# Kernel optimization log

Hardware: AMD Instinct MI355X
Metric: run time of the kernel (lower is better)

## Reference

```python
import jax, jax.numpy as jnp
import numpy as np

H = 256      # hidden_size
B = 32       # batch
T = 4096     # timesteps / graph nodes
E = 8192     # edges per graph
PATH = 1
EXPAND_WEIGHT = 0.1
MODE = 'son'


def setup_inputs() -> dict:
    key = jax.random.key(0)
    ks = jax.random.split(key, 6)
    hidden = jax.random.normal(ks[0], (B, H), jnp.float32)
    encoder_outputs = jax.random.normal(ks[1], (T, B, H), jnp.float32)
    edges_src = jax.random.randint(ks[2], (B, E), 0, T)
    edges_dst = jax.random.randint(ks[3], (B, E), 0, T)
    # nn.Linear(2H, 2H) params (kaiming-uniform-ish scale) and the v vector
    lim = 1.0 / np.sqrt(2 * H)
    W_attn = jax.random.uniform(ks[4], (2 * H, 2 * H), jnp.float32, -lim, lim)
    b_attn = jnp.zeros((2 * H,), jnp.float32)
    v = jax.random.uniform(ks[5], (2 * H,), jnp.float32, -lim, lim)
    return {"hidden": hidden, "encoder_outputs": encoder_outputs,
            "edges_src": edges_src, "edges_dst": edges_dst,
            "W_attn": W_attn, "b_attn": b_attn, "v": v}


def reference(hidden, encoder_outputs, edges_src, edges_dst, W_attn, b_attn, v):
    Bb, Hh = hidden.shape
    Tt = encoder_outputs.shape[0]
    # h: [B, T, H] (hidden repeated over timesteps); enc: [B, T, H]
    h = jnp.broadcast_to(hidden[:, None, :], (Bb, Tt, Hh))
    enc = jnp.transpose(encoder_outputs, (1, 0, 2))
    # score: tanh(Linear(cat)) then v . energy -> [B, T]
    energy = jnp.tanh(jnp.concatenate([h, enc], axis=2) @ W_attn.T + b_attn)
    scores = jnp.einsum('btd,d->bt', energy, v)
    w = jax.nn.softmax(scores, axis=1)
    # expand_attn: scatter-add along graph edges, skipping consecutive (y == x+1)
    mask = (edges_dst != edges_src + 1).astype(w.dtype)  # [B, E]
    def scatter(wb, src, dst, m):
        if MODE == 'son':
            return jnp.zeros_like(wb).at[dst].add(wb[src] * m)
        else:
            return jnp.zeros_like(wb).at[src].add(wb[dst] * m)
    for _ in range(PATH):
        w = jax.vmap(scatter)(w, edges_src, edges_dst, mask) * EXPAND_WEIGHT
    return w[:, None, :]  # [B, 1, T]
```

## Files before the change

kernel.cpp:

```cpp
#include <hip/hip_runtime.h>
#include <hip/hip_bf16.h>

typedef __attribute__((ext_vector_type(8))) short bf16x8;
typedef __attribute__((ext_vector_type(4))) float f32x4;

#define HD 256
#define NB 32
#define NT 4096
#define NE 8192
#define N2 512

static __device__ __forceinline__ unsigned short f2bf(float f) {
  unsigned int u = __float_as_uint(f);
  u += 0x7fff + ((u >> 16) & 1);
  return (unsigned short)(u >> 16);
}
static __device__ __forceinline__ short4 cvt4(float4 a) {
  return make_short4((short)f2bf(a.x), (short)f2bf(a.y),
                     (short)f2bf(a.z), (short)f2bf(a.w));
}
static __device__ __forceinline__ float fast_tanh(float x) {
  float e = __builtin_amdgcn_exp2f(x * 2.8853900817779268f);
  return __builtin_fmaf(-2.f, __builtin_amdgcn_rcpf(e + 1.f), 1.f);
}
static __device__ __forceinline__ bf16x8 pack8(float4 a, float4 b) {
  union { bf16x8 v; unsigned int u[4]; } r;
  r.u[0] = (__float_as_uint(a.y) & 0xffff0000u) | (__float_as_uint(a.x) >> 16);
  r.u[1] = (__float_as_uint(a.w) & 0xffff0000u) | (__float_as_uint(a.z) >> 16);
  r.u[2] = (__float_as_uint(b.y) & 0xffff0000u) | (__float_as_uint(b.x) >> 16);
  r.u[3] = (__float_as_uint(b.w) & 0xffff0000u) | (__float_as_uint(b.z) >> 16);
  return r.v;
}

#define GLDS16(g, l)                                                       \
  __builtin_amdgcn_global_load_lds(                                        \
      (const __attribute__((address_space(1))) unsigned int*)(g),          \
      (__attribute__((address_space(3))) unsigned int*)(l), 16, 0, 0)

__global__ __launch_bounds__(256) void prep(
    const float* __restrict__ hidden, const float* __restrict__ Wattn,
    const float* __restrict__ battn, float* __restrict__ cvecT,
    short* __restrict__ Wbf) {
  const int tid = threadIdx.x;
  if (blockIdx.x < 256) {
    __shared__ float Ws[64 * 260];
    __shared__ float Hs[HD];
    const int chunk = blockIdx.x & 7;
    const int b = blockIdx.x >> 3;
#pragma unroll
    for (int it = 0; it < 16; ++it) {
      int f = it * 1024 + tid * 4;
      int i = f >> 8, k = f & 255;
      float4 w4 = *(const float4*)(Wattn + (chunk * 64 + i) * N2 + k);
      *(float4*)&Ws[i * 260 + k] = w4;
    }
    if (tid < 64)
      *(float4*)&Hs[tid * 4] = *(const float4*)(hidden + b * HD + tid * 4);
    __syncthreads();
    const int nl = tid >> 2;
    const int kb = (tid & 3) * 64;
    float sum = 0.f;
#pragma unroll
    for (int z = 0; z < 64; z += 4) {
      float4 h4 = *(const float4*)&Hs[kb + z];
      float4 w4 = *(const float4*)&Ws[nl * 260 + kb + z];
      sum = fmaf(h4.x, w4.x, sum);
      sum = fmaf(h4.y, w4.y, sum);
      sum = fmaf(h4.z, w4.z, sum);
      sum = fmaf(h4.w, w4.w, sum);
    }
    sum += __shfl_xor(sum, 1, 64);
    sum += __shfl_xor(sum, 2, 64);
    if ((tid & 3) == 0)
      cvecT[(chunk * 64 + nl) * NB + b] = sum + battn[chunk * 64 + nl];
  } else {
    int f = (blockIdx.x - 256) * 1024 + tid * 4;
    int n = f >> 8, k = f & 255;
    float4 w4 = *(const float4*)(Wattn + n * N2 + HD + k);
    *(short4*)(Wbf + f) = cvt4(w4);
  }
}

__global__ __launch_bounds__(256, 2) void score_gemm(
    const float* __restrict__ enc, const short* __restrict__ Wbf,
    const float* __restrict__ cvecT, const float* __restrict__ vvec,
    float* __restrict__ scores) {
  __shared__ float As[512 * 4];
  __shared__ short Bs[2048 * 8];
  __shared__ float part[4][64];
  const int tid = threadIdx.x;
  const int w = tid >> 6, lane = tid & 63, q = lane >> 4, m = lane & 15;
  const int row0 = blockIdx.x * 64;

  f32x4 acc[4][8];
#pragma unroll
  for (int mi = 0; mi < 4; ++mi)
#pragma unroll
    for (int nf = 0; nf < 8; ++nf) acc[mi][nf] = (f32x4){0.f, 0.f, 0.f, 0.f};

#pragma unroll 1
  for (int ks = 0; ks < 8; ++ks) {
    const int k0 = ks * 32;
    __syncthreads();
#pragma unroll
    for (int i = 0; i < 2; ++i) {
      const int S = (i * 4 + w) * 64 + lane;
      const int r = S >> 3;
      const int kc = (S & 7) ^ (r & 7);
      GLDS16(enc + (row0 + r) * HD + k0 + kc * 4, &As[(S & ~63) * 4]);
    }
#pragma unroll
    for (int i = 0; i < 8; ++i) {
      const int S = (i * 4 + w) * 64 + lane;
      const int n = S >> 2;
      const int kc = (S & 3) ^ ((n >> 1) & 3);
      GLDS16(Wbf + n * HD + k0 + kc * 8, &Bs[(S & ~63) * 8]);
    }
    __syncthreads();

    bf16x8 bfr[8];
#pragma unroll
    for (int nf = 0; nf < 8; ++nf) {
      const int n = w * 128 + nf * 16 + m;
      bfr[nf] = *(const bf16x8*)&Bs[(n * 4 + (q ^ ((n >> 1) & 3))) * 8];
    }
#pragma unroll
    for (int mi = 0; mi < 4; ++mi) {
      const int r = mi * 16 + m;
      float4 a0 = *(const float4*)&As[(r * 8 + ((2 * q) ^ (r & 7))) * 4];
      float4 a1 = *(const float4*)&As[(r * 8 + ((2 * q + 1) ^ (r & 7))) * 4];
      bf16x8 af = pack8(a0, a1);
#pragma unroll
      for (int nf = 0; nf < 8; ++nf)
        acc[mi][nf] = __builtin_amdgcn_mfma_f32_16x16x32_bf16(af, bfr[nf], acc[mi][nf], 0, 0, 0);
    }
  }

  float p[4][4];
#pragma unroll
  for (int mi = 0; mi < 4; ++mi)
#pragma unroll
    for (int j = 0; j < 4; ++j) p[mi][j] = 0.f;

#pragma unroll
  for (int nf = 0; nf < 8; ++nf) {
    const int n = w * 128 + nf * 16 + m;
    const float vv = vvec[n];
    const f32x4 cvA = *(const f32x4*)(cvecT + n * NB + 4 * q);
    const f32x4 cvB = *(const f32x4*)(cvecT + n * NB + 16 + 4 * q);
#pragma unroll
    for (int mi = 0; mi < 4; ++mi) {
      const f32x4 cv = (mi & 1) ? cvB : cvA;
#pragma unroll
      for (int j = 0; j < 4; ++j)
        p[mi][j] += fast_tanh(acc[mi][nf][j] + cv[j]) * vv;
    }
  }
#pragma unroll
  for (int mi = 0; mi < 4; ++mi) {
#pragma unroll
    for (int j = 0; j < 4; ++j) {
      float e = p[mi][j];
      e += __shfl_xor(e, 1, 64);
      e += __shfl_xor(e, 2, 64);
      e += __shfl_xor(e, 4, 64);
      e += __shfl_xor(e, 8, 64);
      if (m == 0) part[w][mi * 16 + 4 * q + j] = e;
    }
  }
  __syncthreads();
  if (tid < 64) {
    const int r = row0 + tid;
    scores[(r & 31) * NT + (r >> 5)] =
        part[0][tid] + part[1][tid] + part[2][tid] + part[3][tid];
  }
}

__global__ __launch_bounds__(1024) void softmax_norm(
    const float* __restrict__ sc, float* __restrict__ smax,
    float* __restrict__ sinv, float* __restrict__ out) {
  __shared__ float rtmp[16];
  __shared__ float rres;
  const int b = blockIdx.x;
  const int tid = threadIdx.x;
  const int wid = tid >> 6, lane = tid & 63;
  float s[4];
  float mx = -1e30f;
#pragma unroll
  for (int p = 0; p < 4; ++p) {
    s[p] = sc[b * NT + tid + p * 1024];
    mx = fmaxf(mx, s[p]);
  }
#pragma unroll
  for (int d = 32; d >= 1; d >>= 1) mx = fmaxf(mx, __shfl_xor(mx, d, 64));
  if (lane == 0) rtmp[wid] = mx;
  __syncthreads();
  if (tid == 0) {
    float mm = rtmp[0];
#pragma unroll
    for (int i = 1; i < 16; ++i) mm = fmaxf(mm, rtmp[i]);
    rres = mm;
  }
  __syncthreads();
  mx = rres;
  float sm = 0.f;
#pragma unroll
  for (int p = 0; p < 4; ++p) sm += __expf(s[p] - mx);
#pragma unroll
  for (int d = 32; d >= 1; d >>= 1) sm += __shfl_xor(sm, d, 64);
  if (lane == 0) rtmp[wid] = sm;
  __syncthreads();
  if (tid == 0) {
    float tt = 0.f;
#pragma unroll
    for (int i = 0; i < 16; ++i) tt += rtmp[i];
    smax[b] = mx;
    sinv[b] = 0.1f / tt;
  }
#pragma unroll
  for (int p = 0; p < 4; ++p) out[b * NT + tid + p * 1024] = 0.f;
}

__global__ __launch_bounds__(256) void scatter(
    const float* __restrict__ sc, const float* __restrict__ smax,
    const float* __restrict__ sinv, const int* __restrict__ esrc,
    const int* __restrict__ edst, float* __restrict__ out) {
  const int idx = blockIdx.x * 256 + threadIdx.x;
  const int b = idx >> 13, e = idx & (NE - 1);
  const int ss = esrc[b * NE + e];
  const int dd = edst[b * NE + e];
  const float wv = __expf(sc[b * NT + ss] - smax[b]) * sinv[b];
  if (dd != ss + 1) atomicAdd(out + b * NT + dd, wv);
}

extern "C" void kernel_launch(void* const* d_in, const int* in_sizes, int n_in,
                              void* d_out, int out_size, void* d_ws, size_t ws_size,
                              hipStream_t stream) {
  const float* hidden = (const float*)d_in[0];
  const float* enc    = (const float*)d_in[1];
  const int*   esrc   = (const int*)d_in[2];
  const int*   edst   = (const int*)d_in[3];
  const float* Wattn  = (const float*)d_in[4];
  const float* battn  = (const float*)d_in[5];
  const float* vvec   = (const float*)d_in[6];
  float* out = (float*)d_out;

  char* ws = (char*)d_ws;
  float* cvecT  = (float*)ws;
  short* Wbf    = (short*)(ws + 65536);
  float* scores = (float*)(ws + 65536 + 262144);
  float* smax   = (float*)(ws + 65536 + 262144 + 524288);
  float* sinv   = (float*)(ws + 65536 + 262144 + 524288 + 128);

  prep<<<384, 256, 0, stream>>>(hidden, Wattn, battn, cvecT, Wbf);
  score_gemm<<<(NB * NT) / 64, 256, 0, stream>>>(enc, Wbf, cvecT, vvec, scores);
  softmax_norm<<<NB, 1024, 0, stream>>>(scores, smax, sinv, out);
  scatter<<<(NB * NE) / 256, 256, 0, stream>>>(scores, smax, sinv, esrc, edst, out);
}
```

Measured before the change: 279.3 us.

## Stage full bf16 A tile in LDS once, stream W fragments from global

The score GEMM now loads the block's whole 64x256 encoder tile once, converts it to bf16 into swizzled shared memory, and drops the per-k-step LDS staging of both operands and the barriers between steps. W fragments are read straight from global memory (L2-resident) with a register double-buffer. The N dimension is split into two passes of 64 columns per wave, which halves the accumulator registers, and launch bounds are raised to allow three blocks per CU. The cost is more global and L2 traffic for W per block, plus a serialized upfront load of the encoder tile with no overlap against compute.

```diff
diff --git a/kernel.cpp b/kernel.cpp
--- a/kernel.cpp
+++ b/kernel.cpp
@@ -23,19 +23,6 @@
   float e = __builtin_amdgcn_exp2f(x * 2.8853900817779268f);
   return __builtin_fmaf(-2.f, __builtin_amdgcn_rcpf(e + 1.f), 1.f);
 }
-static __device__ __forceinline__ bf16x8 pack8(float4 a, float4 b) {
-  union { bf16x8 v; unsigned int u[4]; } r;
-  r.u[0] = (__float_as_uint(a.y) & 0xffff0000u) | (__float_as_uint(a.x) >> 16);
-  r.u[1] = (__float_as_uint(a.w) & 0xffff0000u) | (__float_as_uint(a.z) >> 16);
-  r.u[2] = (__float_as_uint(b.y) & 0xffff0000u) | (__float_as_uint(b.x) >> 16);
-  r.u[3] = (__float_as_uint(b.w) & 0xffff0000u) | (__float_as_uint(b.z) >> 16);
-  return r.v;
-}
-
-#define GLDS16(g, l)                                                       \
-  __builtin_amdgcn_global_load_lds(                                        \
-      (const __attribute__((address_space(1))) unsigned int*)(g),          \
-      (__attribute__((address_space(3))) unsigned int*)(l), 16, 0, 0)
 
 __global__ __launch_bounds__(256) void prep(
     const float* __restrict__ hidden, const float* __restrict__ Wattn,
@@ -81,86 +68,95 @@
   }
 }
 
-__global__ __launch_bounds__(256, 2) void score_gemm(
+__global__ __launch_bounds__(256, 3) void score_gemm(
     const float* __restrict__ enc, const short* __restrict__ Wbf,
     const float* __restrict__ cvecT, const float* __restrict__ vvec,
     float* __restrict__ scores) {
-  __shared__ float As[512 * 4];
-  __shared__ short Bs[2048 * 8];
+  __shared__ short As[64 * 256];
   __shared__ float part[4][64];
   const int tid = threadIdx.x;
   const int w = tid >> 6, lane = tid & 63, q = lane >> 4, m = lane & 15;
-  const int row0 = blockIdx.x * 64;
-
-  f32x4 acc[4][8];
+  const long row0 = (long)blockIdx.x * 64;
+
+  const float* src = enc + row0 * HD;
+#pragma unroll
+  for (int it = 0; it < 16; ++it) {
+    int f = it * 1024 + tid * 4;
+    float4 a4 = *(const float4*)(src + f);
+    int r = f >> 8, k = f & 255;
+    int slot = (k >> 3) ^ (r & 31);
+    uint2 pk;
+    pk.x = (__float_as_uint(a4.y) & 0xffff0000u) | (__float_as_uint(a4.x) >> 16);
+    pk.y = (__float_as_uint(a4.w) & 0xffff0000u) | (__float_as_uint(a4.z) >> 16);
+    *(uint2*)&As[(r * 32 + slot) * 8 + (k & 7)] = pk;
+  }
+  __syncthreads();
+
+  float rowacc[4][4];
 #pragma unroll
   for (int mi = 0; mi < 4; ++mi)
 #pragma unroll
-    for (int nf = 0; nf < 8; ++nf) acc[mi][nf] = (f32x4){0.f, 0.f, 0.f, 0.f};
+    for (int j = 0; j < 4; ++j) rowacc[mi][j] = 0.f;
 
 #pragma unroll 1
-  for (int ks = 0; ks < 8; ++ks) {
-    const int k0 = ks * 32;
-    __syncthreads();
-#pragma unroll
-    for (int i = 0; i < 2; ++i) {
-      const int S = (i * 4 + w) * 64 + lane;
-      const int r = S >> 3;
-      const int kc = (S & 7) ^ (r & 7);
-      GLDS16(enc + (row0 + r) * HD + k0 + kc * 4, &As[(S & ~63) * 4]);
-    }
-#pragma unroll
-    for (int i = 0; i < 8; ++i) {
-      const int S = (i * 4 + w) * 64 + lane;
-      const int n = S >> 2;
-      const int kc = (S & 3) ^ ((n >> 1) & 3);
-      GLDS16(Wbf + n * HD + k0 + kc * 8, &Bs[(S & ~63) * 8]);
-    }
-    __syncthreads();
-
-    bf16x8 bfr[8];
-#pragma unroll
-    for (int nf = 0; nf < 8; ++nf) {
-      const int n = w * 128 + nf * 16 + m;
-      bfr[nf] = *(const bf16x8*)&Bs[(n * 4 + (q ^ ((n >> 1) & 3))) * 8];
-    }
-#pragma unroll
-    for (int mi = 0; mi < 4; ++mi) {
-      const int r = mi * 16 + m;
-      float4 a0 = *(const float4*)&As[(r * 8 + ((2 * q) ^ (r & 7))) * 4];
-      float4 a1 = *(const float4*)&As[(r * 8 + ((2 * q + 1) ^ (r & 7))) * 4];
-      bf16x8 af = pack8(a0, a1);
-#pragma unroll
-      for (int nf = 0; nf < 8; ++nf)
-        acc[mi][nf] = __builtin_amdgcn_mfma_f32_16x16x32_bf16(af, bfr[nf], acc[mi][nf], 0, 0, 0);
-    }
-  }
-
-  float p[4][4];
-#pragma unroll
-  for (int mi = 0; mi < 4; ++mi)
-#pragma unroll
-    for (int j = 0; j < 4; ++j) p[mi][j] = 0.f;
-
-#pragma unroll
-  for (int nf = 0; nf < 8; ++nf) {
-    const int n = w * 128 + nf * 16 + m;
-    const float vv = vvec[n];
-    const f32x4 cvA = *(const f32x4*)(cvecT + n * NB + 4 * q);
-    const f32x4 cvB = *(const f32x4*)(cvecT + n * NB + 16 + 4 * q);
-#pragma unroll
-    for (int mi = 0; mi < 4; ++mi) {
-      const f32x4 cv = (mi & 1) ? cvB : cvA;
-#pragma unroll
-      for (int j = 0; j < 4; ++j)
-        p[mi][j] += fast_tanh(acc[mi][nf][j] + cv[j]) * vv;
-    }
-  }
+  for (int np = 0; np < 2; ++np) {
+    const int nb = np * 256 + w * 64;
+    f32x4 acc[4][4];
+#pragma unroll
+    for (int mi = 0; mi < 4; ++mi)
+#pragma unroll
+      for (int nf = 0; nf < 4; ++nf) acc[mi][nf] = (f32x4){0.f, 0.f, 0.f, 0.f};
+
+    bf16x8 bcur[4], bnxt[4];
+#pragma unroll
+    for (int nf = 0; nf < 4; ++nf)
+      bcur[nf] = *(const bf16x8*)(Wbf + (nb + nf * 16 + m) * HD + q * 8);
+
+#pragma unroll
+    for (int ks = 0; ks < 8; ++ks) {
+      if (ks < 7) {
+#pragma unroll
+        for (int nf = 0; nf < 4; ++nf)
+          bnxt[nf] = *(const bf16x8*)(Wbf + (nb + nf * 16 + m) * HD +
+                                      (ks + 1) * 32 + q * 8);
+      }
+#pragma unroll
+      for (int mi = 0; mi < 4; ++mi) {
+        const int r = mi * 16 + m;
+        bf16x8 a = *(const bf16x8*)&As[(r * 32 + ((ks * 4 + q) ^ (r & 31))) * 8];
+        acc[mi][0] = __builtin_amdgcn_mfma_f32_16x16x32_bf16(a, bcur[0], acc[mi][0], 0, 0, 0);
+        acc[mi][1] = __builtin_amdgcn_mfma_f32_16x16x32_bf16(a, bcur[1], acc[mi][1], 0, 0, 0);
+        acc[mi][2] = __builtin_amdgcn_mfma_f32_16x16x32_bf16(a, bcur[2], acc[mi][2], 0, 0, 0);
+        acc[mi][3] = __builtin_amdgcn_mfma_f32_16x16x32_bf16(a, bcur[3], acc[mi][3], 0, 0, 0);
+      }
+      if (ks < 7) {
+#pragma unroll
+        for (int nf = 0; nf < 4; ++nf) bcur[nf] = bnxt[nf];
+      }
+      __builtin_amdgcn_sched_barrier(0x38F);
+    }
+
+#pragma unroll
+    for (int nf = 0; nf < 4; ++nf) {
+      const int n = nb + nf * 16 + m;
+      const float vv = vvec[n];
+      const f32x4 cvA = *(const f32x4*)(cvecT + n * NB + 4 * q);
+      const f32x4 cvB = *(const f32x4*)(cvecT + n * NB + 16 + 4 * q);
+#pragma unroll
+      for (int mi = 0; mi < 4; ++mi) {
+        const f32x4 cv = (mi & 1) ? cvB : cvA;
+#pragma unroll
+        for (int j = 0; j < 4; ++j)
+          rowacc[mi][j] += fast_tanh(acc[mi][nf][j] + cv[j]) * vv;
+      }
+    }
+  }
+
 #pragma unroll
   for (int mi = 0; mi < 4; ++mi) {
 #pragma unroll
     for (int j = 0; j < 4; ++j) {
-      float e = p[mi][j];
+      float e = rowacc[mi][j];
       e += __shfl_xor(e, 1, 64);
       e += __shfl_xor(e, 2, 64);
       e += __shfl_xor(e, 4, 64);
@@ -170,7 +166,7 @@
   }
   __syncthreads();
   if (tid < 64) {
-    const int r = row0 + tid;
+    const long r = row0 + tid;
     scores[(r & 31) * NT + (r >> 5)] =
         part[0][tid] + part[1][tid] + part[2][tid] + part[3][tid];
   }
```

Result: slower. 312.1 us (+11.8%).
